# Optimization experiments

Hardware: AMD Instinct MI355X
Metric: run time of the kernel (lower is better)

The kernel has to match this reference:

```python
import jax, jax.numpy as jnp
import numpy as np

H, DH, ITERS, EPS, LN_EPS = 8, 32, 3, 1e-8, 1e-5

def _ln(x, w, b):
    m = jnp.mean(x, axis=-1, keepdims=True)
    v = jnp.mean(jnp.square(x - m), axis=-1, keepdims=True)
    return (x - m) * jax.lax.rsqrt(v + LN_EPS) * w + b

def setup_inputs() -> dict:
    key = jax.random.key(0)
    ks = jax.random.split(key, 16)
    B, N, D, S = 64, 4096, 256, 8
    DI = H * DH  # 256
    HID = max(D, 128)
    s = 0.02
    return {
        "inputs": jax.random.normal(ks[0], (B, N, D), jnp.float32),
        "noise": jax.random.normal(ks[1], (B, S, D), jnp.float32),
        "slots_mean": jax.random.normal(ks[2], (1, 1, D), jnp.float32),
        "slots_logvar": jax.random.normal(ks[3], (1, 1, D), jnp.float32) * s,
        "wq": jax.random.normal(ks[4], (D, DI), jnp.float32) * s,
        "bq": jnp.zeros((DI,), jnp.float32),
        "wk": jax.random.normal(ks[5], (D, DI), jnp.float32) * s,
        "bk": jnp.zeros((DI,), jnp.float32),
        "wv": jax.random.normal(ks[6], (D, DI), jnp.float32) * s,
        "bv": jnp.zeros((DI,), jnp.float32),
        "wo": jax.random.normal(ks[7], (DI, D), jnp.float32) * s,
        "bo": jnp.zeros((D,), jnp.float32),
        "w_ih": jax.random.normal(ks[8], (D, 3 * D), jnp.float32) * s,
        "b_ih": jnp.zeros((3 * D,), jnp.float32),
        "w_hh": jax.random.normal(ks[9], (D, 3 * D), jnp.float32) * s,
        "b_hh": jnp.zeros((3 * D,), jnp.float32),
        "w1": jax.random.normal(ks[10], (D, HID), jnp.float32) * s,
        "b1": jnp.zeros((HID,), jnp.float32),
        "w2": jax.random.normal(ks[11], (HID, D), jnp.float32) * s,
        "b2": jnp.zeros((D,), jnp.float32),
        "ln_in_w": jnp.ones((D,), jnp.float32), "ln_in_b": jnp.zeros((D,), jnp.float32),
        "ln_s_w": jnp.ones((D,), jnp.float32), "ln_s_b": jnp.zeros((D,), jnp.float32),
        "ln_ff_w": jnp.ones((D,), jnp.float32), "ln_ff_b": jnp.zeros((D,), jnp.float32),
    }

def reference(inputs, noise, slots_mean, slots_logvar, wq, bq, wk, bk, wv, bv,
              wo, bo, w_ih, b_ih, w_hh, b_hh, w1, b1, w2, b2,
              ln_in_w, ln_in_b, ln_s_w, ln_s_b, ln_ff_w, ln_ff_b):
    B, N, D = inputs.shape
    S = noise.shape[1]
    scale = D ** -0.5  # note: scale uses dim, per original code
    # slot init: mean + exp(logvar) * noise (faithful: exp(logvar) used directly)
    slots = slots_mean + jnp.exp(slots_logvar) * noise  # [B,S,D]
    x = _ln(inputs, ln_in_w, ln_in_b)
    k = (x @ wk + bk).reshape(B, N, H, DH).transpose(0, 2, 1, 3)  # [B,H,N,Dh]
    v = (x @ wv + bv).reshape(B, N, H, DH).transpose(0, 2, 1, 3)
    attn = None
    for _ in range(ITERS):
        slots_prev = slots
        s = _ln(slots, ln_s_w, ln_s_b)
        q = (s @ wq + bq).reshape(B, S, H, DH).transpose(0, 2, 1, 3)  # [B,H,S,Dh]
        dots = jnp.einsum('bhid,bhjd->bhij', q, k) * scale  # [B,H,S,N]
        attn = jax.nn.softmax(dots, axis=-2)  # softmax over slot axis
        attn = attn + EPS
        attn = attn / jnp.clip(jnp.sum(attn, axis=-1, keepdims=True), 1e-12)  # L1 over inputs
        upd = jnp.einsum('bhjd,bhij->bhid', v, attn)  # [B,H,S,Dh]
        upd = upd.transpose(0, 2, 1, 3).reshape(B, S, H * DH) @ wo + bo  # [B,S,D]
        # GRUCell (torch gate order r,z,n)
        xg = upd.reshape(B * S, D) @ w_ih + b_ih
        hg = slots_prev.reshape(B * S, D) @ w_hh + b_hh
        xr, xz, xn = jnp.split(xg, 3, axis=-1)
        hr, hz, hn = jnp.split(hg, 3, axis=-1)
        r = jax.nn.sigmoid(xr + hr)
        z = jax.nn.sigmoid(xz + hz)
        n = jnp.tanh(xn + r * hn)
        slots = ((1.0 - z) * n + z * slots_prev.reshape(B * S, D)).reshape(B, S, D)
        ff = _ln(slots, ln_ff_w, ln_ff_b)
        slots = slots + (jax.nn.relu(ff @ w1 + b1) @ w2 + b2)
    return slots, attn
```

## Files before the change

kernel.cpp:

```cpp
#include <hip/hip_runtime.h>
#include <stdint.h>

typedef __attribute__((ext_vector_type(8))) short bf16x8;
typedef __attribute__((ext_vector_type(4))) float f32x4;

__device__ __forceinline__ float b2f(unsigned short s) {
    unsigned int u = ((unsigned int)s) << 16;
    return __builtin_bit_cast(float, u);
}
__device__ __forceinline__ unsigned short f2b(float f) {
    unsigned int u = __builtin_bit_cast(unsigned int, f);
    u += 0x7FFFu + ((u >> 16) & 1u);
    return (unsigned short)(u >> 16);
}
__device__ __forceinline__ void unpack8(uint4 u, float* o) {
    unsigned int a0 = u.x, a1 = u.y, a2 = u.z, a3 = u.w;
    o[0] = __builtin_bit_cast(float, a0 << 16);
    o[1] = __builtin_bit_cast(float, a0 & 0xffff0000u);
    o[2] = __builtin_bit_cast(float, a1 << 16);
    o[3] = __builtin_bit_cast(float, a1 & 0xffff0000u);
    o[4] = __builtin_bit_cast(float, a2 << 16);
    o[5] = __builtin_bit_cast(float, a2 & 0xffff0000u);
    o[6] = __builtin_bit_cast(float, a3 << 16);
    o[7] = __builtin_bit_cast(float, a3 & 0xffff0000u);
}

#define GLOAD_LDS16(g, l) __builtin_amdgcn_global_load_lds( \
    (const __attribute__((address_space(1))) unsigned int*)(g), \
    (__attribute__((address_space(3))) unsigned int*)(l), 16, 0, 0)

#define EPS_ATTN 1e-8f
#define LN_EPS 1e-5f
#define SCALE 0.0625f

__global__ __launch_bounds__(256) void k_prep(const float* __restrict__ wk,
                                              const float* __restrict__ wv,
                                              unsigned short* __restrict__ W3) {
    int g = blockIdx.x * 256 + threadIdx.x;
    int j = g & 7;
    int f = (g >> 3) & 1023;
    int stage = g >> 13;
    int p = f & 15, qq = (f >> 4) & 3, ntl = f >> 6;
    int kc = stage >> 1, half = stage & 1;
    int k = kc * 32 + qq * 8 + j;
    int n = half * 256 + ntl * 16 + p;
    float v = (n < 256) ? wk[k * 256 + n] : wv[k * 256 + (n - 256)];
    W3[g] = f2b(v);
}

__global__ __launch_bounds__(256) void k_init(const float* __restrict__ sm,
                                              const float* __restrict__ slv,
                                              const float* __restrict__ noise,
                                              float* __restrict__ slots) {
    int idx = blockIdx.x * 256 + threadIdx.x;
    int d = idx & 255;
    slots[idx] = sm[d] + expf(slv[d]) * noise[idx];
}

__global__ __launch_bounds__(256, 2) void k_kv(
    const float* __restrict__ x, const float* __restrict__ lnw, const float* __restrict__ lnb,
    const unsigned short* __restrict__ W3, const float* __restrict__ bk, const float* __restrict__ bv,
    unsigned short* __restrict__ Kb, unsigned short* __restrict__ Vb) {
    __shared__ __align__(16) unsigned short sh[33792];
    unsigned short* As = sh;
    unsigned short* Bs = sh + 16384;
    float* bL = (float*)(sh + 32768);
    int t = threadIdx.x;
    int w = t >> 6, lane = t & 63;
    int p = lane & 15, q = lane >> 4;

    {
        const unsigned short* gp = W3 + (size_t)(w * 4) * 512 + lane * 8;
        #pragma unroll
        for (int c = 0; c < 4; ++c)
            GLOAD_LDS16(gp + c * 512, Bs + (w * 4 + c) * 512);
    }
    if (t < 128) {
        float4 bb = (t < 64) ? ((const float4*)bk)[t] : ((const float4*)bv)[t - 64];
        *(float4*)&bL[t * 4] = bb;
    }

    float4 lw  = ((const float4*)lnw)[lane];
    float4 lbv = ((const float4*)lnb)[lane];
    float4 xv[16];
    const float* xbase = x + ((size_t)blockIdx.x * 64 + w * 16) * 256;
    #pragma unroll
    for (int i = 0; i < 16; ++i) xv[i] = ((const float4*)(xbase + i * 256))[lane];
    int kcw = lane >> 3, qw = (lane >> 1) & 3, j0 = (lane & 1) * 4;
    #pragma unroll
    for (int i = 0; i < 16; ++i) {
        float4 v = xv[i];
        float s0 = v.x + v.y + v.z + v.w;
        float s1 = v.x * v.x + v.y * v.y + v.z * v.z + v.w * v.w;
        #pragma unroll
        for (int o = 1; o < 64; o <<= 1) { s0 += __shfl_xor(s0, o); s1 += __shfl_xor(s1, o); }
        float mean = s0 * (1.0f / 256.0f);
        float var  = s1 * (1.0f / 256.0f) - mean * mean;
        float rstd = rsqrtf(var + LN_EPS);
        ushort4 pk;
        pk.x = f2b((v.x - mean) * rstd * lw.x + lbv.x);
        pk.y = f2b((v.y - mean) * rstd * lw.y + lbv.y);
        pk.z = f2b((v.z - mean) * rstd * lw.z + lbv.z);
        pk.w = f2b((v.w - mean) * rstd * lw.w + lbv.w);
        int pos = (qw * 16 + i) ^ kcw;
        *(ushort4*)&As[((w * 8 + kcw) * 64 + pos) * 8 + j0] = pk;
    }
    __syncthreads();

    f32x4 acc[32];
    f32x4 zero = {0.f, 0.f, 0.f, 0.f};
    #pragma unroll
    for (int i = 0; i < 32; ++i) acc[i] = zero;

    for (int s1 = 0; s1 < 16; ++s1) {
        if (s1 < 15) {
            int nx = s1 + 1;
            const unsigned short* gp = W3 + (size_t)nx * 8192 + (w * 4) * 512 + lane * 8;
            unsigned short* lb = Bs + ((nx & 1) ? 8192 : 0);
            #pragma unroll
            for (int c = 0; c < 4; ++c)
                GLOAD_LDS16(gp + c * 512, lb + (w * 4 + c) * 512);
        }
        int kc = s1 >> 1, half = s1 & 1;
        bf16x8 af = *(const bf16x8*)&As[((w * 8 + kc) * 64 + ((q * 16 + p) ^ kc)) * 8];
        const unsigned short* bbuf = Bs + ((s1 & 1) ? 8192 : 0);
        #pragma unroll
        for (int ntl = 0; ntl < 16; ++ntl) {
            bf16x8 bf = *(const bf16x8*)&bbuf[ntl * 512 + lane * 8];
            acc[half * 16 + ntl] = __builtin_amdgcn_mfma_f32_16x16x32_bf16(
                af, bf, acc[half * 16 + ntl], 0, 0, 0);
        }
        __syncthreads();
    }

    unsigned short* rep = As;
    int b_   = blockIdx.x >> 6;
    int n0g  = (blockIdx.x & 63) * 64;
    #pragma unroll
    for (int hf = 0; hf < 2; ++hf) {
        if (hf) __syncthreads();
        #pragma unroll
        for (int al = 0; al < 16; ++al) {
            int ai = hf * 16 + al;
            float bias = bL[hf * 256 + al * 16 + p];
            int hl = al >> 1, dh = (al & 1) * 16 + p;
            #pragma unroll
            for (int r = 0; r < 4; ++r) {
                int nl = w * 16 + q * 4 + r;
                rep[(hl * 64 + nl) * 32 + dh] = f2b(acc[ai][r] + bias);
            }
        }
        __syncthreads();
        unsigned short* dst = hf ? Vb : Kb;
        #pragma unroll
        for (int i = 0; i < 8; ++i) {
            uint4 vd = *(const uint4*)&rep[(i * 256 + t) * 8];
            *(uint4*)(dst + (((size_t)b_ * 8 + i) * 4096 + n0g) * 32 + t * 8) = vd;
        }
    }
}

__global__ __launch_bounds__(256) void k_q(
    const float* __restrict__ slots, const float* __restrict__ lnw, const float* __restrict__ lnb,
    const float* __restrict__ wq, const float* __restrict__ bq, float* __restrict__ qg) {
    __shared__ float sln[256];
    __shared__ float red[8];
    int t = threadIdx.x;
    int row = blockIdx.x;
    float v = slots[(size_t)row * 256 + t];
    float s0 = v, s1 = v * v;
    #pragma unroll
    for (int off = 1; off < 64; off <<= 1) { s0 += __shfl_xor(s0, off); s1 += __shfl_xor(s1, off); }
    if ((t & 63) == 0) { red[t >> 6] = s0; red[4 + (t >> 6)] = s1; }
    __syncthreads();
    float ts0 = red[0] + red[1] + red[2] + red[3];
    float ts1 = red[4] + red[5] + red[6] + red[7];
    float mean = ts0 * (1.f / 256.f);
    float var  = ts1 * (1.f / 256.f) - mean * mean;
    float rstd = rsqrtf(var + LN_EPS);
    sln[t] = (v - mean) * rstd * lnw[t] + lnb[t];
    __syncthreads();
    float acc = bq[t];
    #pragma unroll 4
    for (int k = 0; k < 256; ++k) acc += sln[k] * wq[k * 256 + t];
    int b = row >> 3, sl = row & 7;
    qg[(size_t)b * 2048 + (t >> 5) * 256 + sl * 32 + (t & 31)] = acc;
}

__global__ __launch_bounds__(256, 3) void k_attn(
    const unsigned short* __restrict__ Kg, const unsigned short* __restrict__ Vg,
    const float* __restrict__ qg, float* __restrict__ upd_raw, float* __restrict__ rowsum,
    float* __restrict__ attn_out, int last) {
    __shared__ __align__(16) float VL[256 * 33];
    __shared__ __align__(16) float aL[8 * 264];
    __shared__ float qL[256];
    int t = threadIdx.x;
    int bh = blockIdx.x >> 3;
    int n0 = (blockIdx.x & 7) * 512;
    qL[t] = qg[bh * 256 + t];
    int s2 = t >> 5, dq = (t >> 2) & 7, jp = t & 3;
    float4 uacc = {0.f, 0.f, 0.f, 0.f};
    float rs_loc[8];
    #pragma unroll
    for (int s = 0; s < 8; ++s) rs_loc[s] = 0.f;
    __syncthreads();

    for (int st = 0; st < 2; ++st) {
        int n = n0 + st * 256 + t;
        size_t base = ((size_t)bh * 4096 + n) * 32;
        const uint4* kp = (const uint4*)(Kg + base);
        float kf[32];
        unpack8(kp[0], kf + 0); unpack8(kp[1], kf + 8);
        unpack8(kp[2], kf + 16); unpack8(kp[3], kf + 24);
        float sd[8];
        #pragma unroll
        for (int s = 0; s < 8; ++s) {
            float a = 0.f;
            #pragma unroll
            for (int d4 = 0; d4 < 8; ++d4) {
                float4 q4 = *(const float4*)&qL[s * 32 + d4 * 4];
                a = fmaf(kf[d4 * 4 + 0], q4.x, a);
                a = fmaf(kf[d4 * 4 + 1], q4.y, a);
                a = fmaf(kf[d4 * 4 + 2], q4.z, a);
                a = fmaf(kf[d4 * 4 + 3], q4.w, a);
            }
            sd[s] = a * SCALE;
        }
        float m = sd[0];
        #pragma unroll
        for (int s = 1; s < 8; ++s) m = fmaxf(m, sd[s]);
        float e[8]; float sum = 0.f;
        #pragma unroll
        for (int s = 0; s < 8; ++s) { e[s] = __expf(sd[s] - m); sum += e[s]; }
        float inv = 1.0f / sum;
        float a8[8];
        #pragma unroll
        for (int s = 0; s < 8; ++s) { a8[s] = e[s] * inv + EPS_ATTN; rs_loc[s] += a8[s]; }
        if (last) {
            #pragma unroll
            for (int s = 0; s < 8; ++s)
                attn_out[((size_t)bh * 8 + s) * 4096 + n] = a8[s];
        }
        if (st) __syncthreads();
        #pragma unroll
        for (int s = 0; s < 8; ++s) aL[s * 264 + t] = a8[s];
        const uint4* vp = (const uint4*)(Vg + base);
        float vf[32];
        unpack8(vp[0], vf + 0); unpack8(vp[1], vf + 8);
        unpack8(vp[2], vf + 16); unpack8(vp[3], vf + 24);
        #pragma unroll
        for (int d = 0; d < 32; ++d) VL[t * 33 + d] = vf[d];
        __syncthreads();
        #pragma unroll 4
        for (int j2 = 0; j2 < 64; ++j2) {
            int j = j2 * 4 + jp;
            float av = aL[s2 * 264 + j];
            int vb = j * 33 + dq * 4;
            uacc.x = fmaf(av, VL[vb + 0], uacc.x);
            uacc.y = fmaf(av, VL[vb + 1], uacc.y);
            uacc.z = fmaf(av, VL[vb + 2], uacc.z);
            uacc.w = fmaf(av, VL[vb + 3], uacc.w);
        }
    }
    uacc.x += __shfl_xor(uacc.x, 1); uacc.x += __shfl_xor(uacc.x, 2);
    uacc.y += __shfl_xor(uacc.y, 1); uacc.y += __shfl_xor(uacc.y, 2);
    uacc.z += __shfl_xor(uacc.z, 1); uacc.z += __shfl_xor(uacc.z, 2);
    uacc.w += __shfl_xor(uacc.w, 1); uacc.w += __shfl_xor(uacc.w, 2);
    if (jp == 0) {
        float* up = upd_raw + bh * 256 + s2 * 32 + dq * 4;
        atomicAdd(up + 0, uacc.x);
        atomicAdd(up + 1, uacc.y);
        atomicAdd(up + 2, uacc.z);
        atomicAdd(up + 3, uacc.w);
    }
    #pragma unroll
    for (int s = 0; s < 8; ++s) {
        float v = rs_loc[s];
        #pragma unroll
        for (int o = 1; o < 64; o <<= 1) v += __shfl_xor(v, o);
        if ((t & 63) == 0) atomicAdd(&rowsum[bh * 8 + s], v);
    }
}

__global__ __launch_bounds__(256) void k_gA(
    const float* __restrict__ upd_raw, const float* __restrict__ rowsum,
    const float* __restrict__ wo, const float* __restrict__ bo, float* __restrict__ O) {
    __shared__ float Ul[8][256];
    __shared__ float Pp[4][8][64];
    int t = threadIdx.x;
    int b = blockIdx.x >> 2, cc = blockIdx.x & 3;
    int colbase = cc * 64;
    {
        int r = t >> 5, d0 = (t & 31) * 8;
        int h = d0 >> 5;
        float inv = 1.0f / fmaxf(rowsum[(b * 8 + h) * 8 + r], 1e-12f);
        const float* up = upd_raw + (size_t)(b * 8 + h) * 256 + r * 32 + (d0 & 31);
        float4 u0 = *(const float4*)up;
        float4 u1 = *(const float4*)(up + 4);
        Ul[r][d0 + 0] = u0.x * inv; Ul[r][d0 + 1] = u0.y * inv;
        Ul[r][d0 + 2] = u0.z * inv; Ul[r][d0 + 3] = u0.w * inv;
        Ul[r][d0 + 4] = u1.x * inv; Ul[r][d0 + 5] = u1.y * inv;
        Ul[r][d0 + 6] = u1.z * inv; Ul[r][d0 + 7] = u1.w * inv;
    }
    __syncthreads();
    int c = t & 63, kq = t >> 6;
    float acc[8] = {0.f,0.f,0.f,0.f,0.f,0.f,0.f,0.f};
    const float* wp = wo + (size_t)(kq * 64) * 256 + colbase + c;
    #pragma unroll 16
    for (int k = 0; k < 64; ++k) {
        float wv_ = wp[(size_t)k * 256];
        int kk = kq * 64 + k;
        #pragma unroll
        for (int r = 0; r < 8; ++r) acc[r] += Ul[r][kk] * wv_;
    }
    #pragma unroll
    for (int r = 0; r < 8; ++r) Pp[kq][r][c] = acc[r];
    __syncthreads();
    #pragma unroll
    for (int j = 0; j < 2; ++j) {
        int o = t * 2 + j;
        int r = o >> 6, c2 = o & 63;
        float v = Pp[0][r][c2] + Pp[1][r][c2] + Pp[2][r][c2] + Pp[3][r][c2] + bo[colbase + c2];
        O[(size_t)(b * 8 + r) * 256 + colbase + c2] = v;
    }
}

__global__ __launch_bounds__(256) void k_gB(
    const float* __restrict__ O, const float* __restrict__ slin,
    const float* __restrict__ wih, const float* __restrict__ bih,
    const float* __restrict__ whh, const float* __restrict__ bhh,
    float* __restrict__ gcomb, float* __restrict__ xn, float* __restrict__ hn) {
    __shared__ float Ol[8][256], Hl[8][256];
    __shared__ float Px[2][8][128], Ph[2][8][128];
    int t = threadIdx.x;
    int b = blockIdx.x / 6, cc = blockIdx.x % 6;
    int colbase = cc * 128;
    {
        int r = t >> 5, d0 = (t & 31) * 8;
        const float* op = O + (size_t)(b * 8 + r) * 256 + d0;
        const float* hp = slin + (size_t)(b * 8 + r) * 256 + d0;
        *(float4*)&Ol[r][d0]     = *(const float4*)op;
        *(float4*)&Ol[r][d0 + 4] = *(const float4*)(op + 4);
        *(float4*)&Hl[r][d0]     = *(const float4*)hp;
        *(float4*)&Hl[r][d0 + 4] = *(const float4*)(hp + 4);
    }
    __syncthreads();
    int c = t & 127, kh = t >> 7;
    float ax[8] = {0.f,0.f,0.f,0.f,0.f,0.f,0.f,0.f};
    float ah[8] = {0.f,0.f,0.f,0.f,0.f,0.f,0.f,0.f};
    const float* wxp = wih + (size_t)(kh * 128) * 768 + colbase + c;
    const float* whp = whh + (size_t)(kh * 128) * 768 + colbase + c;
    #pragma unroll 8
    for (int k = 0; k < 128; ++k) {
        float wx = wxp[(size_t)k * 768];
        float wh = whp[(size_t)k * 768];
        int kk = kh * 128 + k;
        #pragma unroll
        for (int r = 0; r < 8; ++r) { ax[r] += Ol[r][kk] * wx; ah[r] += Hl[r][kk] * wh; }
    }
    #pragma unroll
    for (int r = 0; r < 8; ++r) { Px[kh][r][c] = ax[r]; Ph[kh][r][c] = ah[r]; }
    __syncthreads();
    #pragma unroll
    for (int j = 0; j < 4; ++j) {
        int o = t * 4 + j;
        int r = o >> 7, c2 = o & 127;
        int cg = colbase + c2;
        int row = b * 8 + r;
        float vx = Px[0][r][c2] + Px[1][r][c2] + bih[cg];
        float vh = Ph[0][r][c2] + Ph[1][r][c2] + bhh[cg];
        if (cg < 512) {
            gcomb[(size_t)row * 512 + cg] = vx + vh;
        } else {
            xn[(size_t)row * 256 + cg - 512] = vx;
            hn[(size_t)row * 256 + cg - 512] = vh;
        }
    }
}

__global__ __launch_bounds__(256) void k_gC(
    const float* __restrict__ gcomb, const float* __restrict__ xn, const float* __restrict__ hn,
    const float* __restrict__ slin, const float* __restrict__ lnfw, const float* __restrict__ lnfb,
    float* __restrict__ slout, float* __restrict__ F) {
    __shared__ float red[8];
    int t = threadIdx.x, row = blockIdx.x;
    float a_r = gcomb[(size_t)row * 512 + t];
    float a_z = gcomb[(size_t)row * 512 + 256 + t];
    float xnv = xn[(size_t)row * 256 + t];
    float hnv = hn[(size_t)row * 256 + t];
    float hp  = slin[(size_t)row * 256 + t];
    float rg = 1.f / (1.f + expf(-a_r));
    float zg = 1.f / (1.f + expf(-a_z));
    float ng = tanhf(xnv + rg * hnv);
    float s1 = (1.f - zg) * ng + zg * hp;
    slout[(size_t)row * 256 + t] = s1;
    float s0 = s1, sq = s1 * s1;
    #pragma unroll
    for (int o = 1; o < 64; o <<= 1) { s0 += __shfl_xor(s0, o); sq += __shfl_xor(sq, o); }
    if ((t & 63) == 0) { red[t >> 6] = s0; red[4 + (t >> 6)] = sq; }
    __syncthreads();
    float ts0 = red[0] + red[1] + red[2] + red[3];
    float ts1 = red[4] + red[5] + red[6] + red[7];
    float mean = ts0 * (1.f / 256.f);
    float var  = ts1 * (1.f / 256.f) - mean * mean;
    float rstd = rsqrtf(var + LN_EPS);
    F[(size_t)row * 256 + t] = (s1 - mean) * rstd * lnfw[t] + lnfb[t];
}

__global__ __launch_bounds__(256) void k_gD(
    const float* __restrict__ F, const float* __restrict__ w1, const float* __restrict__ b1,
    float* __restrict__ H1) {
    __shared__ float Fl[8][256];
    __shared__ float Pp[4][8][64];
    int t = threadIdx.x;
    int b = blockIdx.x >> 2, cc = blockIdx.x & 3;
    int colbase = cc * 64;
    {
        int r = t >> 5, d0 = (t & 31) * 8;
        const float* fp = F + (size_t)(b * 8 + r) * 256 + d0;
        *(float4*)&Fl[r][d0]     = *(const float4*)fp;
        *(float4*)&Fl[r][d0 + 4] = *(const float4*)(fp + 4);
    }
    __syncthreads();
    int c = t & 63, kq = t >> 6;
    float acc[8] = {0.f,0.f,0.f,0.f,0.f,0.f,0.f,0.f};
    const float* wp = w1 + (size_t)(kq * 64) * 256 + colbase + c;
    #pragma unroll 16
    for (int k = 0; k < 64; ++k) {
        float wv_ = wp[(size_t)k * 256];
        int kk = kq * 64 + k;
        #pragma unroll
        for (int r = 0; r < 8; ++r) acc[r] += Fl[r][kk] * wv_;
    }
    #pragma unroll
    for (int r = 0; r < 8; ++r) Pp[kq][r][c] = acc[r];
    __syncthreads();
    #pragma unroll
    for (int j = 0; j < 2; ++j) {
        int o = t * 2 + j;
        int r = o >> 6, c2 = o & 63;
        float v = Pp[0][r][c2] + Pp[1][r][c2] + Pp[2][r][c2] + Pp[3][r][c2] + b1[colbase + c2];
        H1[(size_t)(b * 8 + r) * 256 + colbase + c2] = fmaxf(v, 0.f);
    }
}

__global__ __launch_bounds__(256) void k_gE(
    const float* __restrict__ H1, const float* __restrict__ w2, const float* __restrict__ b2,
    float* __restrict__ slout) {
    __shared__ float Hl[8][256];
    __shared__ float Pp[4][8][64];
    int t = threadIdx.x;
    int b = blockIdx.x >> 2, cc = blockIdx.x & 3;
    int colbase = cc * 64;
    {
        int r = t >> 5, d0 = (t & 31) * 8;
        const float* hp = H1 + (size_t)(b * 8 + r) * 256 + d0;
        *(float4*)&Hl[r][d0]     = *(const float4*)hp;
        *(float4*)&Hl[r][d0 + 4] = *(const float4*)(hp + 4);
    }
    __syncthreads();
    int c = t & 63, kq = t >> 6;
    float acc[8] = {0.f,0.f,0.f,0.f,0.f,0.f,0.f,0.f};
    const float* wp = w2 + (size_t)(kq * 64) * 256 + colbase + c;
    #pragma unroll 16
    for (int k = 0; k < 64; ++k) {
        float wv_ = wp[(size_t)k * 256];
        int kk = kq * 64 + k;
        #pragma unroll
        for (int r = 0; r < 8; ++r) acc[r] += Hl[r][kk] * wv_;
    }
    #pragma unroll
    for (int r = 0; r < 8; ++r) Pp[kq][r][c] = acc[r];
    __syncthreads();
    #pragma unroll
    for (int j = 0; j < 2; ++j) {
        int o = t * 2 + j;
        int r = o >> 6, c2 = o & 63;
        size_t idx = (size_t)(b * 8 + r) * 256 + colbase + c2;
        float v = Pp[0][r][c2] + Pp[1][r][c2] + Pp[2][r][c2] + Pp[3][r][c2] + b2[colbase + c2];
        slout[idx] = slout[idx] + v;
    }
}

__global__ __launch_bounds__(256) void k_scale(float* __restrict__ attn, const float* __restrict__ rowsum) {
    size_t idx = (size_t)blockIdx.x * 256 + threadIdx.x;
    int row = (int)(idx >> 12);
    float rs = fmaxf(rowsum[row], 1e-12f);
    attn[idx] = attn[idx] / rs;
}

extern "C" void kernel_launch(void* const* d_in, const int* in_sizes, int n_in,
                              void* d_out, int out_size, void* d_ws, size_t ws_size,
                              hipStream_t stream) {
    const float* inputs = (const float*)d_in[0];
    const float* noise  = (const float*)d_in[1];
    const float* sm     = (const float*)d_in[2];
    const float* slv    = (const float*)d_in[3];
    const float* wq     = (const float*)d_in[4];
    const float* bq     = (const float*)d_in[5];
    const float* wk     = (const float*)d_in[6];
    const float* bk     = (const float*)d_in[7];
    const float* wv     = (const float*)d_in[8];
    const float* bv     = (const float*)d_in[9];
    const float* wo     = (const float*)d_in[10];
    const float* bo     = (const float*)d_in[11];
    const float* wih    = (const float*)d_in[12];
    const float* bih    = (const float*)d_in[13];
    const float* whh    = (const float*)d_in[14];
    const float* bhh    = (const float*)d_in[15];
    const float* w1     = (const float*)d_in[16];
    const float* b1     = (const float*)d_in[17];
    const float* w2     = (const float*)d_in[18];
    const float* b2     = (const float*)d_in[19];
    const float* lniw   = (const float*)d_in[20];
    const float* lnib   = (const float*)d_in[21];
    const float* lnsw   = (const float*)d_in[22];
    const float* lnsb   = (const float*)d_in[23];
    const float* lnfw   = (const float*)d_in[24];
    const float* lnfb   = (const float*)d_in[25];

    char* ws = (char*)d_ws;
    unsigned short* Kb = (unsigned short*)ws;
    unsigned short* Vb = (unsigned short*)(ws + 134217728ull);
    float* slotsA  = (float*)(ws + 268435456ull);
    float* slotsB  = (float*)(ws + 268959744ull);
    float* Rr      = (float*)(ws + 269484032ull);
    float* Pr      = (float*)(ws + 270008320ull);
    float* Qr      = (float*)(ws + 270532608ull);
    float* upd_raw = (float*)(ws + 272629760ull);
    float* rowsum  = (float*)(ws + 273154048ull);
    unsigned short* W3 = (unsigned short*)Pr;
    float* O_  = Pr;
    float* gcomb = Qr;
    float* xn = Qr + 262144;
    float* hn = Qr + 393216;
    float* H1 = Qr;
    float* qg = Rr;
    float* F_ = Rr;

    float* out_slots = (float*)d_out;
    float* attn_out  = (float*)d_out + 131072;

    k_prep<<<512, 256, 0, stream>>>(wk, wv, W3);
    k_init<<<512, 256, 0, stream>>>(sm, slv, noise, slotsA);
    k_kv<<<4096, 256, 0, stream>>>(inputs, lniw, lnib, W3, bk, bv, Kb, Vb);
    for (int it = 0; it < 3; ++it) {
        int last = (it == 2);
        float* sl_in  = (it == 0) ? slotsA : ((it == 1) ? slotsB : slotsA);
        float* sl_out = (it == 0) ? slotsB : ((it == 1) ? slotsA : out_slots);
        hipMemsetAsync(upd_raw, 0, 524288 + 16384, stream);
        k_q<<<512, 256, 0, stream>>>(sl_in, lnsw, lnsb, wq, bq, qg);
        k_attn<<<4096, 256, 0, stream>>>(Kb, Vb, qg, upd_raw, rowsum, attn_out, last);
        k_gA<<<256, 256, 0, stream>>>(upd_raw, rowsum, wo, bo, O_);
        k_gB<<<384, 256, 0, stream>>>(O_, sl_in, wih, bih, whh, bhh, gcomb, xn, hn);
        k_gC<<<512, 256, 0, stream>>>(gcomb, xn, hn, sl_in, lnfw, lnfb, sl_out, F_);
        k_gD<<<256, 256, 0, stream>>>(F_, w1, b1, H1);
        k_gE<<<256, 256, 0, stream>>>(H1, w2, b2, sl_out);
    }
    k_scale<<<65536, 256, 0, stream>>>(attn_out, rowsum);
}
```

Measured before the change: 1.221 ms.

## Rewrite slot attention kernel with MFMA and transposed V layout

The attention kernel now computes QK^T and attn·V with bf16 MFMA instructions. Q and the attention weights are split into hi/lo bf16 pairs to keep roughly fp32 accuracy. V is stored transposed by the KV projection kernel so it can feed MFMA directly. Each block handles a full (batch, head) with 8 waves and reduces partial results in LDS, which removes the global atomics and the memset. The trade-offs are extra MFMA passes for the precision split and fewer, larger blocks (512 instead of 4096).

```diff
diff --git a/kernel.cpp b/kernel.cpp
--- a/kernel.cpp
+++ b/kernel.cpp
@@ -136,27 +136,33 @@
     unsigned short* rep = As;
     int b_   = blockIdx.x >> 6;
     int n0g  = (blockIdx.x & 63) * 64;
-    #pragma unroll
-    for (int hf = 0; hf < 2; ++hf) {
-        if (hf) __syncthreads();
-        #pragma unroll
-        for (int al = 0; al < 16; ++al) {
-            int ai = hf * 16 + al;
-            float bias = bL[hf * 256 + al * 16 + p];
-            int hl = al >> 1, dh = (al & 1) * 16 + p;
-            #pragma unroll
-            for (int r = 0; r < 4; ++r) {
-                int nl = w * 16 + q * 4 + r;
-                rep[(hl * 64 + nl) * 32 + dh] = f2b(acc[ai][r] + bias);
-            }
-        }
-        __syncthreads();
-        unsigned short* dst = hf ? Vb : Kb;
-        #pragma unroll
-        for (int i = 0; i < 8; ++i) {
-            uint4 vd = *(const uint4*)&rep[(i * 256 + t) * 8];
-            *(uint4*)(dst + (((size_t)b_ * 8 + i) * 4096 + n0g) * 32 + t * 8) = vd;
-        }
+
+    #pragma unroll
+    for (int al = 0; al < 16; ++al) {
+        float bias = bL[al * 16 + p];
+        int hl = al >> 1, dh = (al & 1) * 16 + p;
+        #pragma unroll
+        for (int r = 0; r < 4; ++r) {
+            int nl = w * 16 + q * 4 + r;
+            rep[(hl * 64 + nl) * 32 + dh] = f2b(acc[al][r] + bias);
+        }
+    }
+    __syncthreads();
+    #pragma unroll
+    for (int i = 0; i < 8; ++i) {
+        uint4 vd = *(const uint4*)&rep[(i * 256 + t) * 8];
+        *(uint4*)(Kb + (((size_t)b_ * 8 + i) * 4096 + n0g) * 32 + t * 8) = vd;
+    }
+    #pragma unroll
+    for (int al = 0; al < 16; ++al) {
+        float bias = bL[256 + al * 16 + p];
+        int hl = al >> 1, dh = (al & 1) * 16 + p;
+        ushort4 pk;
+        pk.x = f2b(acc[16 + al][0] + bias);
+        pk.y = f2b(acc[16 + al][1] + bias);
+        pk.z = f2b(acc[16 + al][2] + bias);
+        pk.w = f2b(acc[16 + al][3] + bias);
+        *(ushort4*)(Vb + ((size_t)(b_ * 8 + hl) * 32 + dh) * 4096 + n0g + w * 16 + q * 4) = pk;
     }
 }
 
@@ -187,98 +193,120 @@
     qg[(size_t)b * 2048 + (t >> 5) * 256 + sl * 32 + (t & 31)] = acc;
 }
 
-__global__ __launch_bounds__(256, 3) void k_attn(
-    const unsigned short* __restrict__ Kg, const unsigned short* __restrict__ Vg,
+__global__ __launch_bounds__(512) void k_attn(
+    const unsigned short* __restrict__ Kg, const unsigned short* __restrict__ VTg,
     const float* __restrict__ qg, float* __restrict__ upd_raw, float* __restrict__ rowsum,
     float* __restrict__ attn_out, int last) {
-    __shared__ __align__(16) float VL[256 * 33];
-    __shared__ __align__(16) float aL[8 * 264];
-    __shared__ float qL[256];
-    int t = threadIdx.x;
-    int bh = blockIdx.x >> 3;
-    int n0 = (blockIdx.x & 7) * 512;
-    qL[t] = qg[bh * 256 + t];
-    int s2 = t >> 5, dq = (t >> 2) & 7, jp = t & 3;
-    float4 uacc = {0.f, 0.f, 0.f, 0.f};
-    float rs_loc[8];
-    #pragma unroll
-    for (int s = 0; s < 8; ++s) rs_loc[s] = 0.f;
-    __syncthreads();
-
-    for (int st = 0; st < 2; ++st) {
-        int n = n0 + st * 256 + t;
-        size_t base = ((size_t)bh * 4096 + n) * 32;
-        const uint4* kp = (const uint4*)(Kg + base);
-        float kf[32];
-        unpack8(kp[0], kf + 0); unpack8(kp[1], kf + 8);
-        unpack8(kp[2], kf + 16); unpack8(kp[3], kf + 24);
-        float sd[8];
-        #pragma unroll
-        for (int s = 0; s < 8; ++s) {
-            float a = 0.f;
-            #pragma unroll
-            for (int d4 = 0; d4 < 8; ++d4) {
-                float4 q4 = *(const float4*)&qL[s * 32 + d4 * 4];
-                a = fmaf(kf[d4 * 4 + 0], q4.x, a);
-                a = fmaf(kf[d4 * 4 + 1], q4.y, a);
-                a = fmaf(kf[d4 * 4 + 2], q4.z, a);
-                a = fmaf(kf[d4 * 4 + 3], q4.w, a);
-            }
-            sd[s] = a * SCALE;
-        }
-        float m = sd[0];
-        #pragma unroll
-        for (int s = 1; s < 8; ++s) m = fmaxf(m, sd[s]);
-        float e[8]; float sum = 0.f;
-        #pragma unroll
-        for (int s = 0; s < 8; ++s) { e[s] = __expf(sd[s] - m); sum += e[s]; }
-        float inv = 1.0f / sum;
-        float a8[8];
-        #pragma unroll
-        for (int s = 0; s < 8; ++s) { a8[s] = e[s] * inv + EPS_ATTN; rs_loc[s] += a8[s]; }
-        if (last) {
-            #pragma unroll
-            for (int s = 0; s < 8; ++s)
-                attn_out[((size_t)bh * 8 + s) * 4096 + n] = a8[s];
-        }
-        if (st) __syncthreads();
-        #pragma unroll
-        for (int s = 0; s < 8; ++s) aL[s * 264 + t] = a8[s];
-        const uint4* vp = (const uint4*)(Vg + base);
-        float vf[32];
-        unpack8(vp[0], vf + 0); unpack8(vp[1], vf + 8);
-        unpack8(vp[2], vf + 16); unpack8(vp[3], vf + 24);
-        #pragma unroll
-        for (int d = 0; d < 32; ++d) VL[t * 33 + d] = vf[d];
-        __syncthreads();
-        #pragma unroll 4
-        for (int j2 = 0; j2 < 64; ++j2) {
-            int j = j2 * 4 + jp;
-            float av = aL[s2 * 264 + j];
-            int vb = j * 33 + dq * 4;
-            uacc.x = fmaf(av, VL[vb + 0], uacc.x);
-            uacc.y = fmaf(av, VL[vb + 1], uacc.y);
-            uacc.z = fmaf(av, VL[vb + 2], uacc.z);
-            uacc.w = fmaf(av, VL[vb + 3], uacc.w);
-        }
-    }
-    uacc.x += __shfl_xor(uacc.x, 1); uacc.x += __shfl_xor(uacc.x, 2);
-    uacc.y += __shfl_xor(uacc.y, 1); uacc.y += __shfl_xor(uacc.y, 2);
-    uacc.z += __shfl_xor(uacc.z, 1); uacc.z += __shfl_xor(uacc.z, 2);
-    uacc.w += __shfl_xor(uacc.w, 1); uacc.w += __shfl_xor(uacc.w, 2);
-    if (jp == 0) {
-        float* up = upd_raw + bh * 256 + s2 * 32 + dq * 4;
-        atomicAdd(up + 0, uacc.x);
-        atomicAdd(up + 1, uacc.y);
-        atomicAdd(up + 2, uacc.z);
-        atomicAdd(up + 3, uacc.w);
-    }
-    #pragma unroll
-    for (int s = 0; s < 8; ++s) {
-        float v = rs_loc[s];
-        #pragma unroll
-        for (int o = 1; o < 64; o <<= 1) v += __shfl_xor(v, o);
-        if ((t & 63) == 0) atomicAdd(&rowsum[bh * 8 + s], v);
+    __shared__ float supd[8][256];
+    __shared__ float srs[8][8];
+    int t = threadIdx.x;
+    int w = t >> 6, lane = t & 63;
+    int c = lane & 15;
+    int g = lane >> 4;
+
+    int bh = blockIdx.x;
+    const unsigned short* Kbh = Kg  + (size_t)bh * 4096 * 32;
+    const unsigned short* Vbh = VTg + (size_t)bh * 32 * 4096;
+
+    bf16x8 qhi = {0,0,0,0,0,0,0,0};
+    bf16x8 qlo = {0,0,0,0,0,0,0,0};
+    if (c < 8) {
+        const float* qp = qg + (size_t)bh * 256 + c * 32 + g * 8;
+        #pragma unroll
+        for (int j = 0; j < 8; ++j) {
+            float qv = qp[j];
+            unsigned short hb = f2b(qv);
+            qhi[j] = (short)hb;
+            qlo[j] = (short)f2b(qv - b2f(hb));
+        }
+    }
+
+    f32x4 zero = {0.f, 0.f, 0.f, 0.f};
+    f32x4 accL = zero, accH = zero;
+    float rs = 0.f;
+    int nb0 = w * 512;
+
+    #pragma unroll 2
+    for (int pr = 0; pr < 16; ++pr) {
+        int base = nb0 + pr * 32;
+        bf16x8 k0 = *(const bf16x8*)(Kbh + (size_t)(base + c) * 32 + g * 8);
+        bf16x8 k1 = *(const bf16x8*)(Kbh + (size_t)(base + 16 + c) * 32 + g * 8);
+        const unsigned short* vlo = Vbh + (size_t)c * 4096 + base + g * 4;
+        const unsigned short* vhi = Vbh + (size_t)(c + 16) * 4096 + base + g * 4;
+        union { ushort4 h[2]; bf16x8 v; } V0, V1;
+        V0.h[0] = *(const ushort4*)vlo;
+        V0.h[1] = *(const ushort4*)(vlo + 16);
+        V1.h[0] = *(const ushort4*)vhi;
+        V1.h[1] = *(const ushort4*)(vhi + 16);
+
+        f32x4 s0 = __builtin_amdgcn_mfma_f32_16x16x32_bf16(k0, qhi, zero, 0, 0, 0);
+        s0 = __builtin_amdgcn_mfma_f32_16x16x32_bf16(k0, qlo, s0, 0, 0, 0);
+        f32x4 s1 = __builtin_amdgcn_mfma_f32_16x16x32_bf16(k1, qhi, zero, 0, 0, 0);
+        s1 = __builtin_amdgcn_mfma_f32_16x16x32_bf16(k1, qlo, s1, 0, 0, 0);
+
+        float d0[4], d1[4];
+        #pragma unroll
+        for (int r = 0; r < 4; ++r) { d0[r] = s0[r] * SCALE; d1[r] = s1[r] * SCALE; }
+        float m = fmaxf(fmaxf(fmaxf(d0[0], d0[1]), fmaxf(d0[2], d0[3])),
+                        fmaxf(fmaxf(d1[0], d1[1]), fmaxf(d1[2], d1[3])));
+        m = fmaxf(m, __shfl_xor(m, 1));
+        m = fmaxf(m, __shfl_xor(m, 2));
+        m = fmaxf(m, __shfl_xor(m, 4));
+        m = fmaxf(m, __shfl_xor(m, 8));
+        float a0[4], a1[4];
+        #pragma unroll
+        for (int r = 0; r < 4; ++r) {
+            float e0 = __expf(d0[r] - m);
+            float e1 = __expf(d1[r] - m);
+            float t0 = e0;
+            t0 += __shfl_xor(t0, 1); t0 += __shfl_xor(t0, 2); t0 += __shfl_xor(t0, 4);
+            float t1 = e1;
+            t1 += __shfl_xor(t1, 1); t1 += __shfl_xor(t1, 2); t1 += __shfl_xor(t1, 4);
+            a0[r] = e0 * (1.0f / t0) + EPS_ATTN;
+            a1[r] = e1 * (1.0f / t1) + EPS_ATTN;
+            rs += a0[r] + a1[r];
+        }
+        if (last && c < 8) {
+            float4 st0 = {a0[0], a0[1], a0[2], a0[3]};
+            float4 st1 = {a1[0], a1[1], a1[2], a1[3]};
+            float* ap = attn_out + ((size_t)bh * 8 + c) * 4096 + base + g * 4;
+            *(float4*)ap = st0;
+            *(float4*)(ap + 16) = st1;
+        }
+        bf16x8 pah, pal;
+        float af[8] = {a0[0], a0[1], a0[2], a0[3], a1[0], a1[1], a1[2], a1[3]};
+        #pragma unroll
+        for (int j = 0; j < 8; ++j) {
+            unsigned short hb = f2b(af[j]);
+            pah[j] = (short)hb;
+            pal[j] = (short)f2b(af[j] - b2f(hb));
+        }
+        accL = __builtin_amdgcn_mfma_f32_16x16x32_bf16(V0.v, pah, accL, 0, 0, 0);
+        accL = __builtin_amdgcn_mfma_f32_16x16x32_bf16(V0.v, pal, accL, 0, 0, 0);
+        accH = __builtin_amdgcn_mfma_f32_16x16x32_bf16(V1.v, pah, accH, 0, 0, 0);
+        accH = __builtin_amdgcn_mfma_f32_16x16x32_bf16(V1.v, pal, accH, 0, 0, 0);
+    }
+
+    rs += __shfl_xor(rs, 16);
+    rs += __shfl_xor(rs, 32);
+    if (lane < 8) srs[w][lane] = rs;
+    if (c < 8) {
+        float* up = &supd[w][c * 32 + g * 4];
+        up[0]  = accL[0]; up[1]  = accL[1]; up[2]  = accL[2]; up[3]  = accL[3];
+        up[16] = accH[0]; up[17] = accH[1]; up[18] = accH[2]; up[19] = accH[3];
+    }
+    __syncthreads();
+    if (t < 256) {
+        float v = 0.f;
+        #pragma unroll
+        for (int ww = 0; ww < 8; ++ww) v += supd[ww][t];
+        upd_raw[(size_t)bh * 256 + t] = v;
+    }
+    if (t < 8) {
+        float v = 0.f;
+        #pragma unroll
+        for (int ww = 0; ww < 8; ++ww) v += srs[ww][t];
+        rowsum[bh * 8 + t] = v;
     }
 }
 
@@ -548,9 +576,8 @@
         int last = (it == 2);
         float* sl_in  = (it == 0) ? slotsA : ((it == 1) ? slotsB : slotsA);
         float* sl_out = (it == 0) ? slotsB : ((it == 1) ? slotsA : out_slots);
-        hipMemsetAsync(upd_raw, 0, 524288 + 16384, stream);
         k_q<<<512, 256, 0, stream>>>(sl_in, lnsw, lnsb, wq, bq, qg);
-        k_attn<<<4096, 256, 0, stream>>>(Kb, Vb, qg, upd_raw, rowsum, attn_out, last);
+        k_attn<<<512, 512, 0, stream>>>(Kb, Vb, qg, upd_raw, rowsum, attn_out, last);
         k_gA<<<256, 256, 0, stream>>>(upd_raw, rowsum, wo, bo, O_);
         k_gB<<<384, 256, 0, stream>>>(O_, sl_in, wih, bih, whh, bhh, gcomb, xn, hn);
         k_gC<<<512, 256, 0, stream>>>(gcomb, xn, hn, sl_in, lnfw, lnfb, sl_out, F_);
```

New measurement: 1.057 ms. 1.15x faster.
